# Optimization experiments

Measured on AMD Instinct MI355X. Metric: run time of the kernel, lower is better.

Reference implementation:

```python
import jax, jax.numpy as jnp
import numpy as np

N_DETS = 16384
DEG = 32
E = N_DETS * DEG
NUM_BLOCKS = 4
SHORTCUT = 128   # shortcutDim
RED = 32         # reducedDim
INNER = 64       # blockInnerDim = 2*32
PW_IN = 9        # pwfeatRawInput
PW_HID = 256     # pwfeatInnerDim
PW_OUT = 32      # pwfeatOutDim


def _xavier(key, shape):
    fan_in, fan_out = shape[-2], shape[-1]
    lim = jnp.sqrt(6.0 / (fan_in + fan_out)).astype(jnp.float32)
    return jax.random.uniform(key, shape, jnp.float32, -lim, lim)


def setup_inputs() -> dict:
    key = jax.random.key(0)
    ks = jax.random.split(key, 24)
    inp = {}
    inp["detFeatures"] = jnp.zeros((N_DETS, SHORTCUT), jnp.float32)
    inp["pairRaw"] = jax.random.normal(ks[0], (E, PW_IN), jnp.float32)
    # every detection has DEG neighbor rows (sorted, all segments non-empty)
    inp["cIdxs"] = jnp.repeat(jnp.arange(N_DETS, dtype=jnp.int32), DEG)
    inp["nIdxs"] = jax.random.randint(ks[1], (E,), 0, N_DETS, jnp.int32)
    # pairwise-feature generator MLP: 9 -> 256 -> 256 -> 32
    inp["g_W1"] = _xavier(ks[2], (PW_IN, PW_HID)); inp["g_b1"] = jnp.zeros((PW_HID,), jnp.float32)
    inp["g_W2"] = _xavier(ks[3], (PW_HID, PW_HID)); inp["g_b2"] = jnp.zeros((PW_HID,), jnp.float32)
    inp["g_W3"] = _xavier(ks[4], (PW_HID, PW_OUT)); inp["g_b3"] = jnp.zeros((PW_OUT,), jnp.float32)
    # per-block params, stacked along leading block dim
    inp["blk_fc1_W"] = _xavier(ks[5], (NUM_BLOCKS, SHORTCUT, RED)); inp["blk_fc1_b"] = jnp.zeros((NUM_BLOCKS, RED), jnp.float32)
    inp["blk_pw_W1"] = _xavier(ks[6], (NUM_BLOCKS, 3 * RED, INNER)); inp["blk_pw_b1"] = jnp.zeros((NUM_BLOCKS, INNER), jnp.float32)
    inp["blk_pw_W2"] = _xavier(ks[7], (NUM_BLOCKS, INNER, INNER)); inp["blk_pw_b2"] = jnp.zeros((NUM_BLOCKS, INNER), jnp.float32)
    inp["blk_post_W1"] = _xavier(ks[8], (NUM_BLOCKS, INNER, INNER)); inp["blk_post_b1"] = jnp.zeros((NUM_BLOCKS, INNER), jnp.float32)
    inp["blk_post_W2"] = _xavier(ks[9], (NUM_BLOCKS, INNER, INNER)); inp["blk_post_b2"] = jnp.zeros((NUM_BLOCKS, INNER), jnp.float32)
    inp["blk_out_W"] = _xavier(ks[10], (NUM_BLOCKS, INNER, SHORTCUT)); inp["blk_out_b"] = jnp.zeros((NUM_BLOCKS, SHORTCUT), jnp.float32)
    inp["s_W"] = _xavier(ks[11], (3, SHORTCUT, SHORTCUT)); inp["s_b"] = jnp.zeros((3, SHORTCUT), jnp.float32)
    inp["pred_W"] = _xavier(ks[12], (SHORTCUT, 1)); inp["pred_b"] = jnp.zeros((1,), jnp.float32)
    return inp


def reference(detFeatures, pairRaw, cIdxs, nIdxs,
              g_W1, g_b1, g_W2, g_b2, g_W3, g_b3,
              blk_fc1_W, blk_fc1_b, blk_pw_W1, blk_pw_b1, blk_pw_W2, blk_pw_b2,
              blk_post_W1, blk_post_b1, blk_post_W2, blk_post_b2,
              blk_out_W, blk_out_b, s_W, s_b, pred_W, pred_b):
    relu = jax.nn.relu
    n_dets = detFeatures.shape[0]
    num_blocks = blk_fc1_W.shape[0]
    # GNet.pairwiseFeaturesFC: pwfeat generator MLP on raw 9-d pair descriptors
    pair = relu(pairRaw @ g_W1 + g_b1)          # (E, 256)
    pair = relu(pair @ g_W2 + g_b2)             # (E, 256)
    pair = relu(pair @ g_W3 + g_b3)             # (E, 32)
    is_id = (cIdxs == nIdxs)[:, None]           # zero-out self-neighbor feats
    x = detFeatures                             # (N, 128)
    for b in range(num_blocks):                 # structurally distinct blocks
        f = relu(x @ blk_fc1_W[b] + blk_fc1_b[b])          # (N, 32)
        cF = f[cIdxs]                                       # (E, 32) gather
        nF = jnp.where(is_id, jnp.float32(0), f[nIdxs])     # (E, 32) gather
        h = jnp.concatenate([pair, cF, nF], axis=1)         # (E, 96)
        h = relu(h @ blk_pw_W1[b] + blk_pw_b1[b])           # (E, 64)
        h = relu(h @ blk_pw_W2[b] + blk_pw_b2[b])           # (E, 64)
        # per-detection max pooling over neighbor rows (segment-max)
        m = jax.ops.segment_max(h, cIdxs, num_segments=n_dets,
                                indices_are_sorted=True)    # (N, 64)
        m = relu(m @ blk_post_W1[b] + blk_post_b1[b])
        m = relu(m @ blk_post_W2[b] + blk_post_b2[b])
        x = relu(x + m @ blk_out_W[b] + blk_out_b[b])        # residual + relu
    for i in range(s_W.shape[0]):
        x = relu(x @ s_W[i] + s_b[i])
    scores = (x @ pred_W + pred_b).reshape(-1)               # (N,)
    return scores
```

## Files before the change

### kernel.cpp

```cpp
#include <hip/hip_runtime.h>

#define N_DETS 16384
#define DEG 32
#define E_EDGES (N_DETS * DEG)
#define EDGE_GRID 512

typedef __attribute__((ext_vector_type(8))) short bf16x8;
typedef __attribute__((ext_vector_type(4))) float f32x4;

__device__ __forceinline__ ushort f32_to_bf16(float v) {
  unsigned u = __float_as_uint(v);
  u += 0x7FFFu + ((u >> 16) & 1u);
  return (ushort)(u >> 16);
}
__device__ __forceinline__ float bf16_to_f32(ushort h) {
  return __uint_as_float((unsigned)h << 16);
}

__global__ __launch_bounds__(256) void split_w_kernel(
    const float* __restrict__ W, ushort* __restrict__ hi, ushort* __restrict__ lo, int N)
{
  const int n = blockIdx.x, k = threadIdx.x;
  const float v = W[(size_t)k * N + n];
  const ushort h = f32_to_bf16(v);
  const ushort l = f32_to_bf16(v - bf16_to_f32(h));
  hi[(size_t)n * 256 + k] = h;
  lo[(size_t)n * 256 + k] = l;
}

__global__ __launch_bounds__(256) void split_edge_w_kernel(
    const float* __restrict__ W1all, const float* __restrict__ W2all,
    ushort* __restrict__ w1h, ushort* __restrict__ w1l,
    ushort* __restrict__ w2h, ushort* __restrict__ w2l)
{
  const int b = blockIdx.x;
  const float* W1 = W1all + b * 6144;
  const float* W2 = W2all + b * 4096;
  for (int i = threadIdx.x; i < 6144; i += 256) {
    const int col = i / 96, k = i % 96;
    const float v = W1[k * 64 + col];
    const ushort h = f32_to_bf16(v);
    w1h[b * 6144 + col * 96 + k] = h;
    w1l[b * 6144 + col * 96 + k] = f32_to_bf16(v - bf16_to_f32(h));
  }
  for (int i = threadIdx.x; i < 4096; i += 256) {
    const int col = i >> 6, k = i & 63;
    const float v = W2[k * 64 + col];
    const ushort h = f32_to_bf16(v);
    w2h[b * 4096 + col * 64 + k] = h;
    w2l[b * 4096 + col * 64 + k] = f32_to_bf16(v - bf16_to_f32(h));
  }
}

__global__ __launch_bounds__(128) void split_score_w_kernel(
    const float* __restrict__ sW, ushort* __restrict__ hi, ushort* __restrict__ lo)
{
  const int layer = blockIdx.x >> 7, col = blockIdx.x & 127, k = threadIdx.x;
  const float v = sW[layer * 16384 + k * 128 + col];
  const ushort h = f32_to_bf16(v);
  hi[layer * 16384 + col * 128 + k] = h;
  lo[layer * 16384 + col * 128 + k] = f32_to_bf16(v - bf16_to_f32(h));
}

#define A_STRIDE 264

__global__ __launch_bounds__(1024, 4) void pair_mlp_kernel(
    const float* __restrict__ raw,
    const float* __restrict__ W1, const float* __restrict__ b1,
    const ushort* __restrict__ w2h, const ushort* __restrict__ w2l,
    const float* __restrict__ b2,
    const ushort* __restrict__ w3h, const ushort* __restrict__ w3l,
    const float* __restrict__ b3,
    ushort* __restrict__ pair_h, ushort* __restrict__ pair_l)
{
  __shared__ __align__(16) ushort ah[64 * A_STRIDE];
  __shared__ __align__(16) ushort al[64 * A_STRIDE];
  __shared__ __align__(16) ushort w3sh[32 * A_STRIDE];
  __shared__ __align__(16) ushort w3sl[32 * A_STRIDE];
  __shared__ __align__(16) float rawt[64 * 12];

  const int t = threadIdx.x;
  const int lane = t & 63, wv = t >> 6;
  const int ln = lane & 15, kg = lane >> 4;

  for (int i = t; i < 32 * 64; i += 1024) {
    const int row = (i * 4) >> 8, col = (i * 4) & 255;
    *(ushort4*)&w3sh[row * A_STRIDE + col] = *(const ushort4*)&w3h[row * 256 + col];
    *(ushort4*)&w3sl[row * A_STRIDE + col] = *(const ushort4*)&w3l[row * 256 + col];
  }

  bf16x8 b2hreg[8], b2lreg[8];
  #pragma unroll
  for (int ks = 0; ks < 8; ++ks) {
    const size_t bo = (size_t)(wv * 16 + ln) * 256 + ks * 32 + kg * 8;
    b2hreg[ks] = *(const bf16x8*)&w2h[bo];
    b2lreg[ks] = *(const bf16x8*)&w2l[bo];
  }
  const float bias2 = b2[wv * 16 + ln];
  const int mt3 = (wv >> 1) & 3, nt3 = wv & 1;
  const float b3v = b3[nt3 * 16 + ln];
  __syncthreads();

  for (int grp = blockIdx.x; grp < E_EDGES / 64; grp += gridDim.x) {
    const long long e0 = (long long)grp * 64;

    if (t < 64 * 9) rawt[(t / 9) * 12 + (t % 9)] = raw[e0 * 9 + t];
    __syncthreads();

    {
      const int col = t & 255, r0 = (t >> 8) * 16;
      const float bv = b1[col];
      float wk[9];
      #pragma unroll
      for (int k = 0; k < 9; ++k) wk[k] = W1[k * 256 + col];
      #pragma unroll
      for (int r = 0; r < 16; ++r) {
        const int row = r0 + r;
        const float4 ra = *(const float4*)&rawt[row * 12];
        const float4 rb = *(const float4*)&rawt[row * 12 + 4];
        const float rc = rawt[row * 12 + 8];
        float s = bv;
        s = fmaf(ra.x, wk[0], s); s = fmaf(ra.y, wk[1], s);
        s = fmaf(ra.z, wk[2], s); s = fmaf(ra.w, wk[3], s);
        s = fmaf(rb.x, wk[4], s); s = fmaf(rb.y, wk[5], s);
        s = fmaf(rb.z, wk[6], s); s = fmaf(rb.w, wk[7], s);
        s = fmaf(rc, wk[8], s);
        const float v = fmaxf(s, 0.f);
        const ushort h = f32_to_bf16(v);
        ah[row * A_STRIDE + col] = h;
        al[row * A_STRIDE + col] = f32_to_bf16(v - bf16_to_f32(h));
      }
    }
    __syncthreads();

    f32x4 acc[4];
    #pragma unroll
    for (int mt = 0; mt < 4; ++mt) {
      acc[mt][0] = 0.f; acc[mt][1] = 0.f; acc[mt][2] = 0.f; acc[mt][3] = 0.f;
    }
    #pragma unroll
    for (int ks = 0; ks < 8; ++ks) {
      const int ka = ks * 32 + kg * 8;
      #pragma unroll
      for (int mt = 0; mt < 4; ++mt) {
        const bf16x8 ahf = *(const bf16x8*)&ah[(mt * 16 + ln) * A_STRIDE + ka];
        const bf16x8 alf = *(const bf16x8*)&al[(mt * 16 + ln) * A_STRIDE + ka];
        acc[mt] = __builtin_amdgcn_mfma_f32_16x16x32_bf16(ahf, b2hreg[ks], acc[mt], 0, 0, 0);
        acc[mt] = __builtin_amdgcn_mfma_f32_16x16x32_bf16(alf, b2hreg[ks], acc[mt], 0, 0, 0);
        acc[mt] = __builtin_amdgcn_mfma_f32_16x16x32_bf16(ahf, b2lreg[ks], acc[mt], 0, 0, 0);
      }
    }
    __syncthreads();

    {
      const int colg = wv * 16 + ln;
      #pragma unroll
      for (int mt = 0; mt < 4; ++mt)
        #pragma unroll
        for (int r = 0; r < 4; ++r) {
          const int rowe = mt * 16 + kg * 4 + r;
          const float v = fmaxf(acc[mt][r] + bias2, 0.f);
          const ushort h = f32_to_bf16(v);
          ah[rowe * A_STRIDE + colg] = h;
          al[rowe * A_STRIDE + colg] = f32_to_bf16(v - bf16_to_f32(h));
        }
    }
    __syncthreads();

    if (wv < 8) {
      f32x4 acc3;
      acc3[0] = 0.f; acc3[1] = 0.f; acc3[2] = 0.f; acc3[3] = 0.f;
      #pragma unroll
      for (int ks = 0; ks < 8; ++ks) {
        const int ka = ks * 32 + kg * 8;
        const bf16x8 a_h = *(const bf16x8*)&ah[(mt3 * 16 + ln) * A_STRIDE + ka];
        const bf16x8 a_l = *(const bf16x8*)&al[(mt3 * 16 + ln) * A_STRIDE + ka];
        const bf16x8 b_h = *(const bf16x8*)&w3sh[(nt3 * 16 + ln) * A_STRIDE + ka];
        const bf16x8 b_l = *(const bf16x8*)&w3sl[(nt3 * 16 + ln) * A_STRIDE + ka];
        acc3 = __builtin_amdgcn_mfma_f32_16x16x32_bf16(a_h, b_h, acc3, 0, 0, 0);
        acc3 = __builtin_amdgcn_mfma_f32_16x16x32_bf16(a_l, b_h, acc3, 0, 0, 0);
        acc3 = __builtin_amdgcn_mfma_f32_16x16x32_bf16(a_h, b_l, acc3, 0, 0, 0);
      }
      const int col3 = nt3 * 16 + ln;
      #pragma unroll
      for (int r = 0; r < 4; ++r) {
        const int rowe = mt3 * 16 + kg * 4 + r;
        const float v = fmaxf(acc3[r] + b3v, 0.f);
        const ushort h = f32_to_bf16(v);
        const size_t idx = (size_t)(e0 + rowe) * 32 + col3;
        pair_h[idx] = h;
        pair_l[idx] = f32_to_bf16(v - bf16_to_f32(h));
      }
    }
    __syncthreads();
  }
}

__global__ __launch_bounds__(256) void fc1_kernel(
    const float* __restrict__ x, const float* __restrict__ W,
    const float* __restrict__ b, float* __restrict__ f,
    ushort* __restrict__ f_h, ushort* __restrict__ f_l)
{
  __shared__ float Wl[128 * 32];
  const int t = threadIdx.x;
  #pragma unroll
  for (int j = 0; j < 4; ++j) {
    const int off = t * 4 + j * 1024;
    *(float4*)&Wl[off] = *(const float4*)&W[off];
  }
  __syncthreads();
  const int c = t & 31, rr = t >> 5;
  const long long r = (long long)blockIdx.x * 8 + rr;
  const float* xr = x + r * 128;
  float acc = b[c];
  #pragma unroll 8
  for (int k = 0; k < 128; k += 4) {
    const float4 a = *(const float4*)&xr[k];
    acc = fmaf(a.x, Wl[(k + 0) * 32 + c], acc);
    acc = fmaf(a.y, Wl[(k + 1) * 32 + c], acc);
    acc = fmaf(a.z, Wl[(k + 2) * 32 + c], acc);
    acc = fmaf(a.w, Wl[(k + 3) * 32 + c], acc);
  }
  const float v = fmaxf(acc, 0.f);
  f[r * 32 + c] = v;
  const ushort h = f32_to_bf16(v);
  f_h[r * 32 + c] = h;
  f_l[r * 32 + c] = f32_to_bf16(v - bf16_to_f32(h));
}

#define W1S 104
#define W2S 72
#define CTS 36

__global__ __launch_bounds__(512, 2) void edge_kernel(
    const ushort* __restrict__ pair_h, const ushort* __restrict__ pair_l,
    const float* __restrict__ f,
    const ushort* __restrict__ f_h, const ushort* __restrict__ f_l,
    const int* __restrict__ nIdxs,
    const float* __restrict__ W1g, const float* __restrict__ bb1,
    const ushort* __restrict__ gw1h, const ushort* __restrict__ gw1l,
    const ushort* __restrict__ gw2h, const ushort* __restrict__ gw2l,
    const float* __restrict__ bb2,
    float* __restrict__ m)
{
  __shared__ __align__(16) ushort W1hS[64 * W1S], W1lS[64 * W1S];
  __shared__ __align__(16) ushort W2hS[64 * W2S], W2lS[64 * W2S];
  __shared__ __align__(16) float  W1cT[64 * CTS];
  __shared__ __align__(16) ushort h1h[8][32 * W2S], h1l[8][32 * W2S];

  const int t = threadIdx.x;
  const int lane = t & 63, wv = t >> 6;
  const int ln = lane & 15, kg = lane >> 4;

  for (int i = t; i < 1536; i += 512) {
    const int idx = i * 4, row = idx / 96, k = idx % 96;
    *(ushort4*)&W1hS[row * W1S + k] = *(const ushort4*)&gw1h[idx];
    *(ushort4*)&W1lS[row * W1S + k] = *(const ushort4*)&gw1l[idx];
  }
  for (int i = t; i < 1024; i += 512) {
    const int idx = i * 4, row = idx >> 6, k = idx & 63;
    *(ushort4*)&W2hS[row * W2S + k] = *(const ushort4*)&gw2h[idx];
    *(ushort4*)&W2lS[row * W2S + k] = *(const ushort4*)&gw2l[idx];
  }
  for (int i = t; i < 2048; i += 512) {
    const int col = i >> 5, j = i & 31;
    W1cT[col * CTS + j] = W1g[(32 + j) * 64 + col];
  }
  __syncthreads();

  for (int dg = blockIdx.x; dg < N_DETS / 8; dg += gridDim.x) {
    const int d = dg * 8 + wv;
    const long long e0 = (long long)d * 32;

    float cfs[4];
    {
      const float4 fv0 = *(const float4*)&f[(size_t)d * 32 + kg * 8];
      const float4 fv1 = *(const float4*)&f[(size_t)d * 32 + kg * 8 + 4];
      #pragma unroll
      for (int nt = 0; nt < 4; ++nt) {
        const int col = nt * 16 + ln;
        const float4 w0 = *(const float4*)&W1cT[col * CTS + kg * 8];
        const float4 w1 = *(const float4*)&W1cT[col * CTS + kg * 8 + 4];
        float s = fv0.x * w0.x + fv0.y * w0.y + fv0.z * w0.z + fv0.w * w0.w
                + fv1.x * w1.x + fv1.y * w1.y + fv1.z * w1.z + fv1.w * w1.w;
        s += __shfl_xor(s, 16);
        s += __shfl_xor(s, 32);
        cfs[nt] = s + bb1[col];
      }
    }

    f32x4 acc1[4][2];
    #pragma unroll
    for (int nt = 0; nt < 4; ++nt)
      #pragma unroll
      for (int mt = 0; mt < 2; ++mt) {
        acc1[nt][mt][0] = 0.f; acc1[nt][mt][1] = 0.f;
        acc1[nt][mt][2] = 0.f; acc1[nt][mt][3] = 0.f;
      }
    bf16x8 ph[2], pl_[2], nh[2], nl_[2];
    #pragma unroll
    for (int mt = 0; mt < 2; ++mt) {
      const long long row = e0 + mt * 16 + ln;
      ph[mt]  = *(const bf16x8*)&pair_h[row * 32 + kg * 8];
      pl_[mt] = *(const bf16x8*)&pair_l[row * 32 + kg * 8];
      const int n = nIdxs[row];
      bf16x8 vh = *(const bf16x8*)&f_h[(size_t)n * 32 + kg * 8];
      bf16x8 vl = *(const bf16x8*)&f_l[(size_t)n * 32 + kg * 8];
      if (n == d) { vh = (bf16x8){0,0,0,0,0,0,0,0}; vl = (bf16x8){0,0,0,0,0,0,0,0}; }
      nh[mt] = vh; nl_[mt] = vl;
    }
    #pragma unroll
    for (int nt = 0; nt < 4; ++nt) {
      const int bro = (nt * 16 + ln) * W1S;
      const bf16x8 b0h = *(const bf16x8*)&W1hS[bro + kg * 8];
      const bf16x8 b0l = *(const bf16x8*)&W1lS[bro + kg * 8];
      const bf16x8 b1h = *(const bf16x8*)&W1hS[bro + 64 + kg * 8];
      const bf16x8 b1l = *(const bf16x8*)&W1lS[bro + 64 + kg * 8];
      #pragma unroll
      for (int mt = 0; mt < 2; ++mt) {
        acc1[nt][mt] = __builtin_amdgcn_mfma_f32_16x16x32_bf16(ph[mt], b0h, acc1[nt][mt], 0, 0, 0);
        acc1[nt][mt] = __builtin_amdgcn_mfma_f32_16x16x32_bf16(pl_[mt], b0h, acc1[nt][mt], 0, 0, 0);
        acc1[nt][mt] = __builtin_amdgcn_mfma_f32_16x16x32_bf16(ph[mt], b0l, acc1[nt][mt], 0, 0, 0);
        acc1[nt][mt] = __builtin_amdgcn_mfma_f32_16x16x32_bf16(nh[mt], b1h, acc1[nt][mt], 0, 0, 0);
        acc1[nt][mt] = __builtin_amdgcn_mfma_f32_16x16x32_bf16(nl_[mt], b1h, acc1[nt][mt], 0, 0, 0);
        acc1[nt][mt] = __builtin_amdgcn_mfma_f32_16x16x32_bf16(nh[mt], b1l, acc1[nt][mt], 0, 0, 0);
      }
    }

    #pragma unroll
    for (int nt = 0; nt < 4; ++nt) {
      const int col = nt * 16 + ln;
      #pragma unroll
      for (int mt = 0; mt < 2; ++mt)
        #pragma unroll
        for (int r = 0; r < 4; ++r) {
          const int row = mt * 16 + kg * 4 + r;
          const float v = fmaxf(acc1[nt][mt][r] + cfs[nt], 0.f);
          const ushort h = f32_to_bf16(v);
          h1h[wv][row * W2S + col] = h;
          h1l[wv][row * W2S + col] = f32_to_bf16(v - bf16_to_f32(h));
        }
    }

    f32x4 acc2[4][2];
    #pragma unroll
    for (int mt = 0; mt < 4; ++mt)
      #pragma unroll
      for (int nt = 0; nt < 2; ++nt) {
        acc2[mt][nt][0] = 0.f; acc2[mt][nt][1] = 0.f;
        acc2[mt][nt][2] = 0.f; acc2[mt][nt][3] = 0.f;
      }
    #pragma unroll
    for (int ks = 0; ks < 2; ++ks) {
      const int ka = ks * 32 + kg * 8;
      bf16x8 bh[2], bl[2];
      #pragma unroll
      for (int nt = 0; nt < 2; ++nt) {
        bh[nt] = *(const bf16x8*)&h1h[wv][(nt * 16 + ln) * W2S + ka];
        bl[nt] = *(const bf16x8*)&h1l[wv][(nt * 16 + ln) * W2S + ka];
      }
      #pragma unroll
      for (int mt = 0; mt < 4; ++mt) {
        const bf16x8 a_h = *(const bf16x8*)&W2hS[(mt * 16 + ln) * W2S + ka];
        const bf16x8 a_l = *(const bf16x8*)&W2lS[(mt * 16 + ln) * W2S + ka];
        #pragma unroll
        for (int nt = 0; nt < 2; ++nt) {
          acc2[mt][nt] = __builtin_amdgcn_mfma_f32_16x16x32_bf16(a_h, bh[nt], acc2[mt][nt], 0, 0, 0);
          acc2[mt][nt] = __builtin_amdgcn_mfma_f32_16x16x32_bf16(a_h, bl[nt], acc2[mt][nt], 0, 0, 0);
          acc2[mt][nt] = __builtin_amdgcn_mfma_f32_16x16x32_bf16(a_l, bh[nt], acc2[mt][nt], 0, 0, 0);
        }
      }
    }

    #pragma unroll
    for (int mt = 0; mt < 4; ++mt)
      #pragma unroll
      for (int r = 0; r < 4; ++r) {
        float mx = fmaxf(acc2[mt][0][r], acc2[mt][1][r]);
        mx = fmaxf(mx, __shfl_xor(mx, 1));
        mx = fmaxf(mx, __shfl_xor(mx, 2));
        mx = fmaxf(mx, __shfl_xor(mx, 4));
        mx = fmaxf(mx, __shfl_xor(mx, 8));
        if (ln == mt * 4 + r) {
          const int outcol = mt * 16 + kg * 4 + r;
          m[(size_t)d * 64 + outcol] = fmaxf(mx + bb2[outcol], 0.f);
        }
      }
  }
}

__global__ __launch_bounds__(256) void post_fused_kernel(
    const float* __restrict__ m, const float* __restrict__ x,
    const float* __restrict__ W1, const float* __restrict__ b1,
    const float* __restrict__ W2, const float* __restrict__ b2,
    const float* __restrict__ Wo, const float* __restrict__ bo,
    float* __restrict__ y)
{
  __shared__ float Wl[64 * 64];
  __shared__ float Wlo[64 * 128];
  __shared__ float mt[32 * 64];
  __shared__ float ht[32 * 64];
  const int t = threadIdx.x;
  const int c = t & 63, g = t >> 6;
  const long long r0 = (long long)blockIdx.x * 32;
  #pragma unroll
  for (int j = 0; j < 4; ++j) {
    const int off = t * 4 + j * 1024;
    *(float4*)&Wl[off] = *(const float4*)&W1[off];
  }
  #pragma unroll
  for (int j = 0; j < 8; ++j) {
    const int off = t * 4 + j * 1024;
    *(float4*)&Wlo[off] = *(const float4*)&Wo[off];
  }
  #pragma unroll
  for (int j = 0; j < 2; ++j) {
    const int off = t * 4 + j * 1024;
    *(float4*)&mt[off] = *(const float4*)&m[r0 * 64 + off];
  }
  __syncthreads();
  float acc[8];
  {
    const float bv = b1[c];
    #pragma unroll
    for (int i = 0; i < 8; ++i) acc[i] = bv;
  }
  #pragma unroll 4
  for (int k = 0; k < 64; k += 4) {
    const float w0 = Wl[(k + 0) * 64 + c], w1 = Wl[(k + 1) * 64 + c];
    const float w2 = Wl[(k + 2) * 64 + c], w3 = Wl[(k + 3) * 64 + c];
    #pragma unroll
    for (int i = 0; i < 8; ++i) {
      const float4 a = *(const float4*)&mt[(g * 8 + i) * 64 + k];
      acc[i] = fmaf(a.x, w0, fmaf(a.y, w1, fmaf(a.z, w2, fmaf(a.w, w3, acc[i]))));
    }
  }
  #pragma unroll
  for (int i = 0; i < 8; ++i) ht[(g * 8 + i) * 64 + c] = fmaxf(acc[i], 0.f);
  __syncthreads();
  #pragma unroll
  for (int j = 0; j < 4; ++j) {
    const int off = t * 4 + j * 1024;
    *(float4*)&Wl[off] = *(const float4*)&W2[off];
  }
  __syncthreads();
  float acc2[8];
  {
    const float bv = b2[c];
    #pragma unroll
    for (int i = 0; i < 8; ++i) acc2[i] = bv;
  }
  #pragma unroll 4
  for (int k = 0; k < 64; k += 4) {
    const float w0 = Wl[(k + 0) * 64 + c], w1 = Wl[(k + 1) * 64 + c];
    const float w2 = Wl[(k + 2) * 64 + c], w3 = Wl[(k + 3) * 64 + c];
    #pragma unroll
    for (int i = 0; i < 8; ++i) {
      const float4 a = *(const float4*)&ht[(g * 8 + i) * 64 + k];
      acc2[i] = fmaf(a.x, w0, fmaf(a.y, w1, fmaf(a.z, w2, fmaf(a.w, w3, acc2[i]))));
    }
  }
  #pragma unroll
  for (int i = 0; i < 8; ++i) mt[(g * 8 + i) * 64 + c] = fmaxf(acc2[i], 0.f);
  __syncthreads();
  const int c2 = t & 127, g2 = t >> 7;
  float acco[16];
  {
    const float bv = bo[c2];
    #pragma unroll
    for (int i = 0; i < 16; ++i) acco[i] = bv;
  }
  #pragma unroll 4
  for (int k = 0; k < 64; k += 4) {
    const float w0 = Wlo[(k + 0) * 128 + c2], w1 = Wlo[(k + 1) * 128 + c2];
    const float w2 = Wlo[(k + 2) * 128 + c2], w3 = Wlo[(k + 3) * 128 + c2];
    #pragma unroll
    for (int i = 0; i < 16; ++i) {
      const float4 a = *(const float4*)&mt[(g2 * 16 + i) * 64 + k];
      acco[i] = fmaf(a.x, w0, fmaf(a.y, w1, fmaf(a.z, w2, fmaf(a.w, w3, acco[i]))));
    }
  }
  #pragma unroll
  for (int i = 0; i < 16; ++i) {
    const long long idx = (r0 + g2 * 16 + i) * 128 + c2;
    y[idx] = fmaxf(x[idx] + acco[i], 0.f);
  }
}

#define XS 136

__global__ __launch_bounds__(512) void score_head_kernel(
    const float* __restrict__ x,
    const ushort* __restrict__ swh, const ushort* __restrict__ swl,
    const float* __restrict__ sb,
    const float* __restrict__ pW, const float* __restrict__ pb,
    float* __restrict__ out)
{
  __shared__ __align__(16) ushort xh[2][32 * XS], xl[2][32 * XS];
  __shared__ __align__(16) float hsf[32 * XS];
  __shared__ float pWs[128];
  const int t = threadIdx.x;
  const int lane = t & 63, wv = t >> 6;
  const int ln = lane & 15, kg = lane >> 4;
  const long long r0 = (long long)blockIdx.x * 32;

  if (t < 128) pWs[t] = pW[t];
  for (int i = t; i < 32 * 32; i += 512) {
    const int row = i >> 5, cq = (i & 31) * 4;
    const float4 v4 = *(const float4*)&x[(r0 + row) * 128 + cq];
    const float vv[4] = {v4.x, v4.y, v4.z, v4.w};
    #pragma unroll
    for (int j = 0; j < 4; ++j) {
      const ushort h = f32_to_bf16(vv[j]);
      xh[0][row * XS + cq + j] = h;
      xl[0][row * XS + cq + j] = f32_to_bf16(vv[j] - bf16_to_f32(h));
    }
  }
  __syncthreads();

  const int colg = wv * 16 + ln;
  int cur = 0;
  #pragma unroll 1
  for (int layer = 0; layer < 3; ++layer) {
    const ushort* wh = swh + (size_t)layer * 16384 + (size_t)colg * 128;
    const ushort* wl = swl + (size_t)layer * 16384 + (size_t)colg * 128;
    f32x4 acc[2];
    #pragma unroll
    for (int mt = 0; mt < 2; ++mt) {
      acc[mt][0] = 0.f; acc[mt][1] = 0.f; acc[mt][2] = 0.f; acc[mt][3] = 0.f;
    }
    #pragma unroll
    for (int ks = 0; ks < 4; ++ks) {
      const int ka = ks * 32 + kg * 8;
      const bf16x8 b_h = *(const bf16x8*)&wh[ka];
      const bf16x8 b_l = *(const bf16x8*)&wl[ka];
      #pragma unroll
      for (int mt = 0; mt < 2; ++mt) {
        const bf16x8 a_h = *(const bf16x8*)&xh[cur][(mt * 16 + ln) * XS + ka];
        const bf16x8 a_l = *(const bf16x8*)&xl[cur][(mt * 16 + ln) * XS + ka];
        acc[mt] = __builtin_amdgcn_mfma_f32_16x16x32_bf16(a_h, b_h, acc[mt], 0, 0, 0);
        acc[mt] = __builtin_amdgcn_mfma_f32_16x16x32_bf16(a_l, b_h, acc[mt], 0, 0, 0);
        acc[mt] = __builtin_amdgcn_mfma_f32_16x16x32_bf16(a_h, b_l, acc[mt], 0, 0, 0);
      }
    }
    const float bias = sb[layer * 128 + colg];
    __syncthreads();
    if (layer < 2) {
      #pragma unroll
      for (int mt = 0; mt < 2; ++mt)
        #pragma unroll
        for (int r = 0; r < 4; ++r) {
          const int row = mt * 16 + kg * 4 + r;
          const float v = fmaxf(acc[mt][r] + bias, 0.f);
          const ushort h = f32_to_bf16(v);
          xh[cur ^ 1][row * XS + colg] = h;
          xl[cur ^ 1][row * XS + colg] = f32_to_bf16(v - bf16_to_f32(h));
        }
      cur ^= 1;
    } else {
      #pragma unroll
      for (int mt = 0; mt < 2; ++mt)
        #pragma unroll
        for (int r = 0; r < 4; ++r) {
          const int row = mt * 16 + kg * 4 + r;
          hsf[row * XS + colg] = fmaxf(acc[mt][r] + bias, 0.f);
        }
    }
    __syncthreads();
  }

  {
    const int row = t >> 4, l16 = t & 15;
    const float4 a0 = *(const float4*)&hsf[row * XS + l16 * 8];
    const float4 a1 = *(const float4*)&hsf[row * XS + l16 * 8 + 4];
    const float4 w0 = *(const float4*)&pWs[l16 * 8];
    const float4 w1 = *(const float4*)&pWs[l16 * 8 + 4];
    float s = a0.x * w0.x + a0.y * w0.y + a0.z * w0.z + a0.w * w0.w
            + a1.x * w1.x + a1.y * w1.y + a1.z * w1.z + a1.w * w1.w;
    s += __shfl_xor(s, 1);
    s += __shfl_xor(s, 2);
    s += __shfl_xor(s, 4);
    s += __shfl_xor(s, 8);
    if (l16 == 0) out[r0 + row] = s + pb[0];
  }
}

extern "C" void kernel_launch(void* const* d_in, const int* in_sizes, int n_in,
                              void* d_out, int out_size, void* d_ws, size_t ws_size,
                              hipStream_t stream)
{
  const float* detF    = (const float*)d_in[0];
  const float* pairRaw = (const float*)d_in[1];
  const int*   cIdx    = (const int*)d_in[2];
  const int*   nIdx    = (const int*)d_in[3];
  const float* gW1 = (const float*)d_in[4];   const float* gb1 = (const float*)d_in[5];
  const float* gW2 = (const float*)d_in[6];   const float* gb2 = (const float*)d_in[7];
  const float* gW3 = (const float*)d_in[8];   const float* gb3 = (const float*)d_in[9];
  const float* fc1W = (const float*)d_in[10]; const float* fc1b = (const float*)d_in[11];
  const float* pwW1 = (const float*)d_in[12]; const float* pwb1 = (const float*)d_in[13];
  const float* pwW2 = (const float*)d_in[14]; const float* pwb2 = (const float*)d_in[15];
  const float* poW1 = (const float*)d_in[16]; const float* pob1 = (const float*)d_in[17];
  const float* poW2 = (const float*)d_in[18]; const float* pob2 = (const float*)d_in[19];
  const float* outW = (const float*)d_in[20]; const float* outb = (const float*)d_in[21];
  const float* sW = (const float*)d_in[22];   const float* sb = (const float*)d_in[23];
  const float* predW = (const float*)d_in[24]; const float* predb = (const float*)d_in[25];
  float* out = (float*)d_out;
  (void)cIdx;

  ushort* w2h  = (ushort*)d_ws;
  ushort* w2l  = w2h + 65536;
  ushort* w3h  = w2l + 65536;
  ushort* w3l  = w3h + 8192;
  ushort* w1eh = w3l + 8192;
  ushort* w1el = w1eh + 24576;
  ushort* w2eh = w1el + 24576;
  ushort* w2el = w2eh + 16384;
  ushort* swh  = w2el + 16384;
  ushort* swl  = swh + 49152;
  ushort* pair_h = swl + 49152;
  ushort* pair_l = pair_h + (size_t)E_EDGES * 32;
  ushort* f_h    = pair_l + (size_t)E_EDGES * 32;
  ushort* f_l    = f_h + (size_t)N_DETS * 32;
  float* f  = (float*)(f_l + (size_t)N_DETS * 32);
  float* m  = f  + (size_t)N_DETS * 32;
  float* mm = m  + (size_t)N_DETS * 64;
  float* xa = mm + (size_t)N_DETS * 64;
  float* xb = xa + (size_t)N_DETS * 128;

  hipMemcpyAsync(xa, detF, (size_t)N_DETS * 128 * sizeof(float),
                 hipMemcpyDeviceToDevice, stream);

  split_w_kernel<<<256, 256, 0, stream>>>(gW2, w2h, w2l, 256);
  split_w_kernel<<<32, 256, 0, stream>>>(gW3, w3h, w3l, 32);
  split_edge_w_kernel<<<4, 256, 0, stream>>>(pwW1, pwW2, w1eh, w1el, w2eh, w2el);
  split_score_w_kernel<<<384, 128, 0, stream>>>(sW, swh, swl);

  pair_mlp_kernel<<<256, 1024, 0, stream>>>(pairRaw, gW1, gb1,
      w2h, w2l, gb2, w3h, w3l, gb3, pair_h, pair_l);

  float* xin = xa;
  float* xout = xb;
  for (int b = 0; b < 4; ++b) {
    fc1_kernel<<<N_DETS / 8, 256, 0, stream>>>(xin, fc1W + b * 4096, fc1b + b * 32,
        f, f_h, f_l);
    edge_kernel<<<EDGE_GRID, 512, 0, stream>>>(pair_h, pair_l, f, f_h, f_l, nIdx,
        pwW1 + b * 6144, pwb1 + b * 64,
        w1eh + b * 6144, w1el + b * 6144, w2eh + b * 4096, w2el + b * 4096,
        pwb2 + b * 64, m);
    post_fused_kernel<<<N_DETS / 32, 256, 0, stream>>>(m, xin,
        poW1 + b * 4096, pob1 + b * 64, poW2 + b * 4096, pob2 + b * 64,
        outW + b * 8192, outb + b * 128, xout);
    float* tmp = xout; xout = xin; xin = tmp;
  }
  score_head_kernel<<<N_DETS / 32, 512, 0, stream>>>(xin, swh, swl, sb,
      predW, predb, out);
}
```

Before: 724.3 us.

## Fuse next block's fc1 into post kernel and move post MLP to split-bf16 MFMA

Rewrites the per-block post MLP (64->64->64->128 plus residual) to use bf16 hi/lo split MFMA instructions instead of scalar fp32 FMAs, with weights pre-split by a new setup kernel. It also fuses the following block's fc1 projection into the tail of the same kernel, so the separate fc1 launch per block and the re-read of x are removed. The split emulates fp32 with three MFMAs per step, which may lose a little precision, and the added register and LDS use could lower occupancy.

```diff
diff --git a/kernel.cpp b/kernel.cpp
--- a/kernel.cpp
+++ b/kernel.cpp
@@ -60,6 +60,42 @@
   const ushort h = f32_to_bf16(v);
   hi[layer * 16384 + col * 128 + k] = h;
   lo[layer * 16384 + col * 128 + k] = f32_to_bf16(v - bf16_to_f32(h));
+}
+
+__global__ __launch_bounds__(256) void split_post_w_kernel(
+    const float* __restrict__ poW1, const float* __restrict__ poW2,
+    const float* __restrict__ outW, const float* __restrict__ fc1W,
+    ushort* __restrict__ p1h, ushort* __restrict__ p1l,
+    ushort* __restrict__ p2h, ushort* __restrict__ p2l,
+    ushort* __restrict__ oh,  ushort* __restrict__ ol,
+    ushort* __restrict__ fh,  ushort* __restrict__ fl)
+{
+  const int b = blockIdx.x;
+  for (int i = threadIdx.x; i < 4096; i += 256) {
+    const int col = i >> 6, k = i & 63;
+    float v = poW1[b * 4096 + k * 64 + col];
+    ushort h = f32_to_bf16(v);
+    p1h[b * 4096 + col * 64 + k] = h;
+    p1l[b * 4096 + col * 64 + k] = f32_to_bf16(v - bf16_to_f32(h));
+    v = poW2[b * 4096 + k * 64 + col];
+    h = f32_to_bf16(v);
+    p2h[b * 4096 + col * 64 + k] = h;
+    p2l[b * 4096 + col * 64 + k] = f32_to_bf16(v - bf16_to_f32(h));
+  }
+  for (int i = threadIdx.x; i < 8192; i += 256) {
+    const int col = i >> 6, k = i & 63;
+    const float v = outW[b * 8192 + k * 128 + col];
+    const ushort h = f32_to_bf16(v);
+    oh[b * 8192 + col * 64 + k] = h;
+    ol[b * 8192 + col * 64 + k] = f32_to_bf16(v - bf16_to_f32(h));
+  }
+  for (int i = threadIdx.x; i < 4096; i += 256) {
+    const int col = i >> 7, k = i & 127;
+    const float v = fc1W[b * 4096 + k * 32 + col];
+    const ushort h = f32_to_bf16(v);
+    fh[b * 4096 + col * 128 + k] = h;
+    fl[b * 4096 + col * 128 + k] = f32_to_bf16(v - bf16_to_f32(h));
+  }
 }
 
 #define A_STRIDE 264
@@ -389,101 +425,166 @@
   }
 }
 
-__global__ __launch_bounds__(256) void post_fused_kernel(
+#define PS 72
+#define PXS 136
+
+__global__ __launch_bounds__(512) void postfc1_kernel(
     const float* __restrict__ m, const float* __restrict__ x,
-    const float* __restrict__ W1, const float* __restrict__ b1,
-    const float* __restrict__ W2, const float* __restrict__ b2,
-    const float* __restrict__ Wo, const float* __restrict__ bo,
-    float* __restrict__ y)
-{
-  __shared__ float Wl[64 * 64];
-  __shared__ float Wlo[64 * 128];
-  __shared__ float mt[32 * 64];
-  __shared__ float ht[32 * 64];
+    const ushort* __restrict__ p1h, const ushort* __restrict__ p1l,
+    const float* __restrict__ pob1,
+    const ushort* __restrict__ p2h, const ushort* __restrict__ p2l,
+    const float* __restrict__ pob2,
+    const ushort* __restrict__ oh, const ushort* __restrict__ ol,
+    const float* __restrict__ outb,
+    const ushort* __restrict__ fch, const ushort* __restrict__ fcl,
+    const float* __restrict__ fcb, int do_fc1,
+    float* __restrict__ y,
+    float* __restrict__ f, ushort* __restrict__ f_h, ushort* __restrict__ f_l)
+{
+  __shared__ __align__(16) ushort mh[32 * PS], ml[32 * PS];
+  __shared__ __align__(16) ushort hh[32 * PS], hl[32 * PS];
+  __shared__ __align__(16) ushort yh[32 * PXS], yl[32 * PXS];
   const int t = threadIdx.x;
-  const int c = t & 63, g = t >> 6;
+  const int lane = t & 63, wv = t >> 6;
+  const int ln = lane & 15, kg = lane >> 4;
   const long long r0 = (long long)blockIdx.x * 32;
-  #pragma unroll
-  for (int j = 0; j < 4; ++j) {
-    const int off = t * 4 + j * 1024;
-    *(float4*)&Wl[off] = *(const float4*)&W1[off];
-  }
-  #pragma unroll
-  for (int j = 0; j < 8; ++j) {
-    const int off = t * 4 + j * 1024;
-    *(float4*)&Wlo[off] = *(const float4*)&Wo[off];
-  }
-  #pragma unroll
-  for (int j = 0; j < 2; ++j) {
-    const int off = t * 4 + j * 1024;
-    *(float4*)&mt[off] = *(const float4*)&m[r0 * 64 + off];
+
+  for (int i = t; i < 32 * 16; i += 512) {
+    const int row = i >> 4, cq = (i & 15) * 4;
+    const float4 v4 = *(const float4*)&m[(r0 + row) * 64 + cq];
+    const float vv[4] = {v4.x, v4.y, v4.z, v4.w};
+    #pragma unroll
+    for (int j = 0; j < 4; ++j) {
+      const ushort h = f32_to_bf16(vv[j]);
+      mh[row * PS + cq + j] = h;
+      ml[row * PS + cq + j] = f32_to_bf16(vv[j] - bf16_to_f32(h));
+    }
   }
   __syncthreads();
-  float acc[8];
+
   {
-    const float bv = b1[c];
-    #pragma unroll
-    for (int i = 0; i < 8; ++i) acc[i] = bv;
-  }
-  #pragma unroll 4
-  for (int k = 0; k < 64; k += 4) {
-    const float w0 = Wl[(k + 0) * 64 + c], w1 = Wl[(k + 1) * 64 + c];
-    const float w2 = Wl[(k + 2) * 64 + c], w3 = Wl[(k + 3) * 64 + c];
-    #pragma unroll
-    for (int i = 0; i < 8; ++i) {
-      const float4 a = *(const float4*)&mt[(g * 8 + i) * 64 + k];
-      acc[i] = fmaf(a.x, w0, fmaf(a.y, w1, fmaf(a.z, w2, fmaf(a.w, w3, acc[i]))));
-    }
-  }
-  #pragma unroll
-  for (int i = 0; i < 8; ++i) ht[(g * 8 + i) * 64 + c] = fmaxf(acc[i], 0.f);
+    const int mt = wv >> 2, nt = wv & 3, col = nt * 16 + ln;
+    const ushort* bh = p1h + (size_t)col * 64;
+    const ushort* bl = p1l + (size_t)col * 64;
+    f32x4 acc; acc[0] = 0.f; acc[1] = 0.f; acc[2] = 0.f; acc[3] = 0.f;
+    #pragma unroll
+    for (int ks = 0; ks < 2; ++ks) {
+      const int ka = ks * 32 + kg * 8;
+      const bf16x8 a_h = *(const bf16x8*)&mh[(mt * 16 + ln) * PS + ka];
+      const bf16x8 a_l = *(const bf16x8*)&ml[(mt * 16 + ln) * PS + ka];
+      const bf16x8 b_h = *(const bf16x8*)&bh[ka];
+      const bf16x8 b_l = *(const bf16x8*)&bl[ka];
+      acc = __builtin_amdgcn_mfma_f32_16x16x32_bf16(a_h, b_h, acc, 0, 0, 0);
+      acc = __builtin_amdgcn_mfma_f32_16x16x32_bf16(a_l, b_h, acc, 0, 0, 0);
+      acc = __builtin_amdgcn_mfma_f32_16x16x32_bf16(a_h, b_l, acc, 0, 0, 0);
+    }
+    const float bias = pob1[col];
+    #pragma unroll
+    for (int r = 0; r < 4; ++r) {
+      const int row = mt * 16 + kg * 4 + r;
+      const float v = fmaxf(acc[r] + bias, 0.f);
+      const ushort h = f32_to_bf16(v);
+      hh[row * PS + col] = h;
+      hl[row * PS + col] = f32_to_bf16(v - bf16_to_f32(h));
+    }
+  }
   __syncthreads();
-  #pragma unroll
-  for (int j = 0; j < 4; ++j) {
-    const int off = t * 4 + j * 1024;
-    *(float4*)&Wl[off] = *(const float4*)&W2[off];
+
+  {
+    const int mt = wv >> 2, nt = wv & 3, col = nt * 16 + ln;
+    const ushort* bh = p2h + (size_t)col * 64;
+    const ushort* bl = p2l + (size_t)col * 64;
+    f32x4 acc; acc[0] = 0.f; acc[1] = 0.f; acc[2] = 0.f; acc[3] = 0.f;
+    #pragma unroll
+    for (int ks = 0; ks < 2; ++ks) {
+      const int ka = ks * 32 + kg * 8;
+      const bf16x8 a_h = *(const bf16x8*)&hh[(mt * 16 + ln) * PS + ka];
+      const bf16x8 a_l = *(const bf16x8*)&hl[(mt * 16 + ln) * PS + ka];
+      const bf16x8 b_h = *(const bf16x8*)&bh[ka];
+      const bf16x8 b_l = *(const bf16x8*)&bl[ka];
+      acc = __builtin_amdgcn_mfma_f32_16x16x32_bf16(a_h, b_h, acc, 0, 0, 0);
+      acc = __builtin_amdgcn_mfma_f32_16x16x32_bf16(a_l, b_h, acc, 0, 0, 0);
+      acc = __builtin_amdgcn_mfma_f32_16x16x32_bf16(a_h, b_l, acc, 0, 0, 0);
+    }
+    const float bias = pob2[col];
+    __syncthreads();
+    #pragma unroll
+    for (int r = 0; r < 4; ++r) {
+      const int row = mt * 16 + kg * 4 + r;
+      const float v = fmaxf(acc[r] + bias, 0.f);
+      const ushort h = f32_to_bf16(v);
+      mh[row * PS + col] = h;
+      ml[row * PS + col] = f32_to_bf16(v - bf16_to_f32(h));
+    }
   }
   __syncthreads();
-  float acc2[8];
+
   {
-    const float bv = b2[c];
-    #pragma unroll
-    for (int i = 0; i < 8; ++i) acc2[i] = bv;
-  }
-  #pragma unroll 4
-  for (int k = 0; k < 64; k += 4) {
-    const float w0 = Wl[(k + 0) * 64 + c], w1 = Wl[(k + 1) * 64 + c];
-    const float w2 = Wl[(k + 2) * 64 + c], w3 = Wl[(k + 3) * 64 + c];
-    #pragma unroll
-    for (int i = 0; i < 8; ++i) {
-      const float4 a = *(const float4*)&ht[(g * 8 + i) * 64 + k];
-      acc2[i] = fmaf(a.x, w0, fmaf(a.y, w1, fmaf(a.z, w2, fmaf(a.w, w3, acc2[i]))));
-    }
-  }
-  #pragma unroll
-  for (int i = 0; i < 8; ++i) mt[(g * 8 + i) * 64 + c] = fmaxf(acc2[i], 0.f);
+    const int col = wv * 16 + ln;
+    const ushort* bh = oh + (size_t)col * 64;
+    const ushort* bl = ol + (size_t)col * 64;
+    f32x4 acc[2];
+    #pragma unroll
+    for (int mt = 0; mt < 2; ++mt) {
+      acc[mt][0] = 0.f; acc[mt][1] = 0.f; acc[mt][2] = 0.f; acc[mt][3] = 0.f;
+    }
+    #pragma unroll
+    for (int ks = 0; ks < 2; ++ks) {
+      const int ka = ks * 32 + kg * 8;
+      const bf16x8 b_h = *(const bf16x8*)&bh[ka];
+      const bf16x8 b_l = *(const bf16x8*)&bl[ka];
+      #pragma unroll
+      for (int mt = 0; mt < 2; ++mt) {
+        const bf16x8 a_h = *(const bf16x8*)&mh[(mt * 16 + ln) * PS + ka];
+        const bf16x8 a_l = *(const bf16x8*)&ml[(mt * 16 + ln) * PS + ka];
+        acc[mt] = __builtin_amdgcn_mfma_f32_16x16x32_bf16(a_h, b_h, acc[mt], 0, 0, 0);
+        acc[mt] = __builtin_amdgcn_mfma_f32_16x16x32_bf16(a_l, b_h, acc[mt], 0, 0, 0);
+        acc[mt] = __builtin_amdgcn_mfma_f32_16x16x32_bf16(a_h, b_l, acc[mt], 0, 0, 0);
+      }
+    }
+    const float bias = outb[col];
+    #pragma unroll
+    for (int mt = 0; mt < 2; ++mt)
+      #pragma unroll
+      for (int r = 0; r < 4; ++r) {
+        const int row = mt * 16 + kg * 4 + r;
+        const size_t idx = (size_t)(r0 + row) * 128 + col;
+        const float v = fmaxf(x[idx] + acc[mt][r] + bias, 0.f);
+        y[idx] = v;
+        const ushort h = f32_to_bf16(v);
+        yh[row * PXS + col] = h;
+        yl[row * PXS + col] = f32_to_bf16(v - bf16_to_f32(h));
+      }
+  }
   __syncthreads();
-  const int c2 = t & 127, g2 = t >> 7;
-  float acco[16];
-  {
-    const float bv = bo[c2];
-    #pragma unroll
-    for (int i = 0; i < 16; ++i) acco[i] = bv;
-  }
-  #pragma unroll 4
-  for (int k = 0; k < 64; k += 4) {
-    const float w0 = Wlo[(k + 0) * 128 + c2], w1 = Wlo[(k + 1) * 128 + c2];
-    const float w2 = Wlo[(k + 2) * 128 + c2], w3 = Wlo[(k + 3) * 128 + c2];
-    #pragma unroll
-    for (int i = 0; i < 16; ++i) {
-      const float4 a = *(const float4*)&mt[(g2 * 16 + i) * 64 + k];
-      acco[i] = fmaf(a.x, w0, fmaf(a.y, w1, fmaf(a.z, w2, fmaf(a.w, w3, acco[i]))));
-    }
-  }
-  #pragma unroll
-  for (int i = 0; i < 16; ++i) {
-    const long long idx = (r0 + g2 * 16 + i) * 128 + c2;
-    y[idx] = fmaxf(x[idx] + acco[i], 0.f);
+
+  if (do_fc1 && wv < 4) {
+    const int mt = wv >> 1, nt = wv & 1, col = nt * 16 + ln;
+    const ushort* bh = fch + (size_t)col * 128;
+    const ushort* bl = fcl + (size_t)col * 128;
+    f32x4 acc; acc[0] = 0.f; acc[1] = 0.f; acc[2] = 0.f; acc[3] = 0.f;
+    #pragma unroll
+    for (int ks = 0; ks < 4; ++ks) {
+      const int ka = ks * 32 + kg * 8;
+      const bf16x8 a_h = *(const bf16x8*)&yh[(mt * 16 + ln) * PXS + ka];
+      const bf16x8 a_l = *(const bf16x8*)&yl[(mt * 16 + ln) * PXS + ka];
+      const bf16x8 b_h = *(const bf16x8*)&bh[ka];
+      const bf16x8 b_l = *(const bf16x8*)&bl[ka];
+      acc = __builtin_amdgcn_mfma_f32_16x16x32_bf16(a_h, b_h, acc, 0, 0, 0);
+      acc = __builtin_amdgcn_mfma_f32_16x16x32_bf16(a_l, b_h, acc, 0, 0, 0);
+      acc = __builtin_amdgcn_mfma_f32_16x16x32_bf16(a_h, b_l, acc, 0, 0, 0);
+    }
+    const float bias = fcb[col];
+    #pragma unroll
+    for (int r = 0; r < 4; ++r) {
+      const int row = mt * 16 + kg * 4 + r;
+      const float v = fmaxf(acc[r] + bias, 0.f);
+      const size_t idx = (size_t)(r0 + row) * 32 + col;
+      f[idx] = v;
+      const ushort h = f32_to_bf16(v);
+      f_h[idx] = h;
+      f_l[idx] = f32_to_bf16(v - bf16_to_f32(h));
+    }
   }
 }
 
@@ -617,14 +718,21 @@
   ushort* w2el = w2eh + 16384;
   ushort* swh  = w2el + 16384;
   ushort* swl  = swh + 49152;
-  ushort* pair_h = swl + 49152;
+  ushort* p1h  = swl + 49152;
+  ushort* p1l  = p1h + 16384;
+  ushort* p2h  = p1l + 16384;
+  ushort* p2l  = p2h + 16384;
+  ushort* ohh  = p2l + 16384;
+  ushort* ohl  = ohh + 32768;
+  ushort* fth  = ohl + 32768;
+  ushort* ftl  = fth + 16384;
+  ushort* pair_h = ftl + 16384;
   ushort* pair_l = pair_h + (size_t)E_EDGES * 32;
   ushort* f_h    = pair_l + (size_t)E_EDGES * 32;
   ushort* f_l    = f_h + (size_t)N_DETS * 32;
   float* f  = (float*)(f_l + (size_t)N_DETS * 32);
   float* m  = f  + (size_t)N_DETS * 32;
-  float* mm = m  + (size_t)N_DETS * 64;
-  float* xa = mm + (size_t)N_DETS * 64;
+  float* xa = m  + (size_t)N_DETS * 64;
   float* xb = xa + (size_t)N_DETS * 128;
 
   hipMemcpyAsync(xa, detF, (size_t)N_DETS * 128 * sizeof(float),
@@ -634,22 +742,28 @@
   split_w_kernel<<<32, 256, 0, stream>>>(gW3, w3h, w3l, 32);
   split_edge_w_kernel<<<4, 256, 0, stream>>>(pwW1, pwW2, w1eh, w1el, w2eh, w2el);
   split_score_w_kernel<<<384, 128, 0, stream>>>(sW, swh, swl);
+  split_post_w_kernel<<<4, 256, 0, stream>>>(poW1, poW2, outW, fc1W,
+      p1h, p1l, p2h, p2l, ohh, ohl, fth, ftl);
 
   pair_mlp_kernel<<<256, 1024, 0, stream>>>(pairRaw, gW1, gb1,
       w2h, w2l, gb2, w3h, w3l, gb3, pair_h, pair_l);
+
+  fc1_kernel<<<N_DETS / 8, 256, 0, stream>>>(xa, fc1W, fc1b, f, f_h, f_l);
 
   float* xin = xa;
   float* xout = xb;
   for (int b = 0; b < 4; ++b) {
-    fc1_kernel<<<N_DETS / 8, 256, 0, stream>>>(xin, fc1W + b * 4096, fc1b + b * 32,
-        f, f_h, f_l);
     edge_kernel<<<EDGE_GRID, 512, 0, stream>>>(pair_h, pair_l, f, f_h, f_l, nIdx,
         pwW1 + b * 6144, pwb1 + b * 64,
         w1eh + b * 6144, w1el + b * 6144, w2eh + b * 4096, w2el + b * 4096,
         pwb2 + b * 64, m);
-    post_fused_kernel<<<N_DETS / 32, 256, 0, stream>>>(m, xin,
-        poW1 + b * 4096, pob1 + b * 64, poW2 + b * 4096, pob2 + b * 64,
-        outW + b * 8192, outb + b * 128, xout);
+    const int nb = (b + 1) & 3;
+    postfc1_kernel<<<N_DETS / 32, 512, 0, stream>>>(m, xin,
+        p1h + b * 4096, p1l + b * 4096, pob1 + b * 64,
+        p2h + b * 4096, p2l + b * 4096, pob2 + b * 64,
+        ohh + b * 8192, ohl + b * 8192, outb + b * 128,
+        fth + nb * 4096, ftl + nb * 4096, fc1b + nb * 32, (b < 3) ? 1 : 0,
+        xout, f, f_h, f_l);
     float* tmp = xout; xout = xin; xin = tmp;
   }
   score_head_kernel<<<N_DETS / 32, 512, 0, stream>>>(xin, swh, swl, sb,
```

After: 678.2 us. -6.4%, faster.
